# Kernel tuning notes

Measured on AMD Instinct MI355X. Metric: run time of the kernel, lower is better.

The kernel has to match this reference:

```python
import jax, jax.numpy as jnp
import numpy as np

H, DI, N, K, R, FF = 2048, 4096, 16, 4, 128, 5632
B, S = 2, 1024
EPS = 1e-6


def rmsnorm(x, w):
    v = jnp.mean(x * x, axis=-1, keepdims=True)
    return x * jax.lax.rsqrt(v + EPS) * w


def setup_inputs() -> dict:
    key = jax.random.key(0)
    ks = jax.random.split(key, 16)
    sc = 0.02
    inp = {
        "hidden_states": jax.random.normal(ks[0], (B, S, H), jnp.float32),
        "input_ln_w": jnp.ones((H,), jnp.float32),
        "w_in": jax.random.normal(ks[1], (2 * DI, H), jnp.float32) * sc,
        "conv_w": jax.random.normal(ks[2], (DI, 1, K), jnp.float32) * 0.3,
        "conv_b": jax.random.normal(ks[3], (DI,), jnp.float32) * sc,
        "w_x": jax.random.normal(ks[4], (R + 2 * N, DI), jnp.float32) * sc,
        "dt_ln_w": jnp.ones((R,), jnp.float32),
        "b_ln_w": jnp.ones((N,), jnp.float32),
        "c_ln_w": jnp.ones((N,), jnp.float32),
        "w_dt": jax.random.normal(ks[5], (DI, R), jnp.float32) * sc,
        "b_dt": jax.random.normal(ks[6], (DI,), jnp.float32) * sc - 4.0,
        "A_log": jnp.broadcast_to(jnp.log(jnp.arange(1, N + 1, dtype=jnp.float32)), (DI, N)),
        "D_skip": jnp.ones((DI,), jnp.float32),
        "w_out": jax.random.normal(ks[7], (H, DI), jnp.float32) * sc,
        "pre_ff_ln_w": jnp.ones((H,), jnp.float32),
        "w_gate": jax.random.normal(ks[8], (FF, H), jnp.float32) * sc,
        "w_up": jax.random.normal(ks[9], (FF, H), jnp.float32) * sc,
        "w_down": jax.random.normal(ks[10], (H, FF), jnp.float32) * sc,
    }
    return inp


def causal_conv1d(x, w, b):
    # x: [B,S,DI], w: [DI,1,K] depthwise, left-pad K-1 (causal)
    y = jax.lax.conv_general_dilated(
        x.transpose(0, 2, 1), w,
        window_strides=(1,), padding=[(K - 1, 0)],
        dimension_numbers=("NCH", "OIH", "NCH"),
        feature_group_count=DI)
    return (y + b[None, :, None]).transpose(0, 2, 1)


def selective_scan(u, A, Bm, Cm, Dp, dt):
    # u,dt: [B,S,DI]; A: [DI,N]; Bm,Cm: [B,S,N]
    def step(h, xs):
        dt_t, B_t, C_t, u_t = xs  # [B,DI],[B,N],[B,N],[B,DI]
        dA = jnp.exp(dt_t[:, :, None] * A)                      # [B,DI,N]
        dBu = dt_t[:, :, None] * B_t[:, None, :] * u_t[:, :, None]
        h = dA * h + dBu
        y = jnp.einsum("bdn,bn->bd", h, C_t)
        return h, y

    xs = (dt.transpose(1, 0, 2), Bm.transpose(1, 0, 2),
          Cm.transpose(1, 0, 2), u.transpose(1, 0, 2))
    h0 = jnp.zeros((u.shape[0], DI, N), u.dtype)
    _, ys = jax.lax.scan(step, h0, xs)
    return ys.transpose(1, 0, 2) + u * Dp  # [B,S,DI]


def reference(hidden_states, input_ln_w, w_in, conv_w, conv_b, w_x, dt_ln_w,
              b_ln_w, c_ln_w, w_dt, b_dt, A_log, D_skip, w_out, pre_ff_ln_w,
              w_gate, w_up, w_down):
    residual = hidden_states
    x = rmsnorm(hidden_states, input_ln_w)

    # --- Mamba mixer ---
    proj = x @ w_in.T                       # [B,S,2*DI]
    u, gate = jnp.split(proj, 2, axis=-1)
    u = jax.nn.silu(causal_conv1d(u, conv_w, conv_b))
    ssm_p = u @ w_x.T                       # [B,S,R+2N]
    t_r, Bm, Cm = jnp.split(ssm_p, [R, R + N], axis=-1)
    t_r = rmsnorm(t_r, dt_ln_w)
    Bm = rmsnorm(Bm, b_ln_w)
    Cm = rmsnorm(Cm, c_ln_w)
    dt = jax.nn.softplus(t_r @ w_dt.T + b_dt)  # [B,S,DI]
    A = -jnp.exp(A_log)
    y = selective_scan(u, A, Bm, Cm, D_skip, dt)
    y = y * jax.nn.silu(gate)
    mixer_out = y @ w_out.T                  # [B,S,H]

    hidden = residual + mixer_out
    residual = hidden
    h = rmsnorm(hidden, pre_ff_ln_w)
    ff = (jax.nn.silu(h @ w_gate.T) * (h @ w_up.T)) @ w_down.T
    return residual + ff
```

## Files before the change

### kernel.cpp

```cpp
#include <hip/hip_runtime.h>
#include <stdint.h>

#define H_   2048
#define DI_  4096
#define N_   16
#define K_   4
#define R_   128
#define FF_  5632
#define B_   2
#define S_   1024
#define MROWS (B_*S_)
#define PCH  16
#define CSTEPS (S_/PCH)

typedef float f32x4 __attribute__((ext_vector_type(4)));
typedef float f32x2 __attribute__((ext_vector_type(2)));
typedef __bf16 bf16x8 __attribute__((ext_vector_type(8)));

__device__ __forceinline__ unsigned short f2bf(float f) {
    union { float f; unsigned u; } v; v.f = f;
    unsigned r = v.u + 0x7fffu + ((v.u >> 16) & 1u);
    return (unsigned short)(r >> 16);
}

__device__ __forceinline__ void gload16(const void* g, void* lds) {
    __builtin_amdgcn_global_load_lds(
        (const __attribute__((address_space(1))) unsigned int*)(uintptr_t)g,
        (__attribute__((address_space(3))) unsigned int*)(unsigned int)(uintptr_t)lds,
        16, 0, 0);
}

__global__ __launch_bounds__(256, 2)
void gemm_bt(const unsigned short* __restrict__ A, const unsigned short* __restrict__ Bt,
             float* __restrict__ C, int M, int N, int K, int Kc)
{
    __shared__ __align__(16) unsigned short As[128 * 64];
    __shared__ __align__(16) unsigned short Bs[128 * 64];
    const int t = threadIdx.x;
    const int l = t & 63;
    const int wv = t >> 6;

    int nwg = gridDim.x * gridDim.y;
    int wg = blockIdx.y * gridDim.x + blockIdx.x;
    if ((nwg & 7) == 0) {
        int q = nwg >> 3;
        wg = (wg & 7) * q + (wg >> 3);
    }
    const int bx = wg % gridDim.x;
    const int by = wg / gridDim.x;
    const long m0 = (long)by * 128;
    const long n0 = (long)bx * 128;
    const int wm = (wv >> 1) * 64;
    const int wn = (wv & 1) * 64;
    const long kstart = (long)blockIdx.z * Kc;
    C += (long)blockIdx.z * M * (long)N;

    f32x4 acc[4][4] = {};

    const int tr = t >> 3;
    const int cs = (t & 7) ^ (tr & 7);
    const unsigned short* gA = A + (m0 + tr) * (long)K + kstart + cs * 8;
    const unsigned short* gB = Bt + (n0 + tr) * (long)K + kstart + cs * 8;
    const unsigned ldsbase = (unsigned)(t & 192) * 16;

    for (int kt = 0; kt < Kc; kt += 64) {
#pragma unroll
        for (int j = 0; j < 4; ++j) {
            gload16(gA + (long)j * 32 * K, (char*)As + j * 4096 + ldsbase);
            gload16(gB + (long)j * 32 * K, (char*)Bs + j * 4096 + ldsbase);
        }
        gA += 64; gB += 64;
        __syncthreads();
#pragma unroll
        for (int k0 = 0; k0 < 2; ++k0) {
            bf16x8 af[4], bfr[4];
#pragma unroll
            for (int i = 0; i < 4; ++i) {
                int rowa = wm + i * 16 + (l & 15);
                int ca = (k0 * 4 + (l >> 4)) ^ (rowa & 7);
                af[i] = *(const bf16x8*)(As + rowa * 64 + ca * 8);
                int rowb = wn + i * 16 + (l & 15);
                int cb = (k0 * 4 + (l >> 4)) ^ (rowb & 7);
                bfr[i] = *(const bf16x8*)(Bs + rowb * 64 + cb * 8);
            }
#pragma unroll
            for (int i = 0; i < 4; ++i)
#pragma unroll
                for (int jn = 0; jn < 4; ++jn)
                    acc[i][jn] = __builtin_amdgcn_mfma_f32_16x16x32_bf16(
                        af[i], bfr[jn], acc[i][jn], 0, 0, 0);
        }
        __syncthreads();
    }

    const int crow = (l >> 4) * 4;
    const int ccol = l & 15;
#pragma unroll
    for (int i = 0; i < 4; ++i) {
#pragma unroll
        for (int jn = 0; jn < 4; ++jn) {
            long row = m0 + wm + i * 16 + crow;
            long col = n0 + wn + jn * 16 + ccol;
            float* cp = C + row * (long)N + col;
#pragma unroll
            for (int q = 0; q < 4; ++q) cp[(long)q * N] = acc[i][jn][q];
        }
    }
}

__global__ __launch_bounds__(512, 1)
void gemm_bt256(const unsigned short* __restrict__ A, const unsigned short* __restrict__ Bt,
                float* __restrict__ C, int M, int N, int K, int Kc)
{
    __shared__ __align__(16) unsigned short As[2][256 * 64];
    __shared__ __align__(16) unsigned short Bs[2][256 * 64];
    const int t = threadIdx.x;
    const int l = t & 63;
    const int wv = t >> 6;
    const int wm = wv >> 2;
    const int wn = wv & 3;

    int nwg = gridDim.x * gridDim.y;
    int wg = blockIdx.y * gridDim.x + blockIdx.x;
    if ((nwg & 7) == 0) {
        int q = nwg >> 3;
        wg = (wg & 7) * q + (wg >> 3);
    }
    const int bx = wg % gridDim.x;
    const int by = wg / gridDim.x;
    const long m0 = (long)by * 256;
    const long n0 = (long)bx * 256;
    const long kstart = (long)blockIdx.z * Kc;
    C += (long)blockIdx.z * M * (long)N;

    f32x4 acc[8][4] = {};

    const int cs = (t & 7) ^ ((t >> 3) & 7);
    const unsigned short* gA = A + (m0 + (t >> 3)) * (long)K + kstart + cs * 8;
    const unsigned short* gB = Bt + (n0 + (t >> 3)) * (long)K + kstart + cs * 8;
    const int NT = Kc >> 6;

#pragma unroll
    for (int i = 0; i < 4; ++i)
        gload16(gA + (long)i * 64 * K, &As[0][t * 8 + i * 4096]);
#pragma unroll
    for (int i = 0; i < 4; ++i)
        gload16(gB + (long)i * 64 * K, &Bs[0][t * 8 + i * 4096]);

    for (int kt = 0; kt < NT; ++kt) {
        const int buf = kt & 1;
        const long koff = (long)((kt + 1 < NT) ? (kt + 1) : kt) * 64;
#pragma unroll
        for (int i = 0; i < 4; ++i)
            gload16(gA + koff + (long)i * 64 * K, &As[buf ^ 1][t * 8 + i * 4096]);
        asm volatile("s_waitcnt vmcnt(4)" ::: "memory");
        __builtin_amdgcn_sched_barrier(0);
        __builtin_amdgcn_s_barrier();
        __builtin_amdgcn_sched_barrier(0);
        {
            bf16x8 af[8], bfr[4];
#pragma unroll
            for (int nf = 0; nf < 4; ++nf) {
                int rowb = wn * 64 + nf * 16 + (l & 15);
                int cb = (l >> 4) ^ (rowb & 7);
                bfr[nf] = *(const bf16x8*)(&Bs[buf][rowb * 64 + cb * 8]);
            }
#pragma unroll
            for (int mf = 0; mf < 8; ++mf) {
                int rowa = wm * 128 + mf * 16 + (l & 15);
                int ca = (l >> 4) ^ (rowa & 7);
                af[mf] = *(const bf16x8*)(&As[buf][rowa * 64 + ca * 8]);
            }
            __builtin_amdgcn_s_setprio(1);
#pragma unroll
            for (int mf = 0; mf < 8; ++mf)
#pragma unroll
                for (int nf = 0; nf < 4; ++nf)
                    acc[mf][nf] = __builtin_amdgcn_mfma_f32_16x16x32_bf16(
                        af[mf], bfr[nf], acc[mf][nf], 0, 0, 0);
            __builtin_amdgcn_s_setprio(0);
        }
        __builtin_amdgcn_sched_barrier(0);
#pragma unroll
        for (int i = 0; i < 4; ++i)
            gload16(gB + koff + (long)i * 64 * K, &Bs[buf ^ 1][t * 8 + i * 4096]);
        {
            bf16x8 af[8], bfr[4];
#pragma unroll
            for (int nf = 0; nf < 4; ++nf) {
                int rowb = wn * 64 + nf * 16 + (l & 15);
                int cb = (4 + (l >> 4)) ^ (rowb & 7);
                bfr[nf] = *(const bf16x8*)(&Bs[buf][rowb * 64 + cb * 8]);
            }
#pragma unroll
            for (int mf = 0; mf < 8; ++mf) {
                int rowa = wm * 128 + mf * 16 + (l & 15);
                int ca = (4 + (l >> 4)) ^ (rowa & 7);
                af[mf] = *(const bf16x8*)(&As[buf][rowa * 64 + ca * 8]);
            }
            __builtin_amdgcn_s_setprio(1);
#pragma unroll
            for (int mf = 0; mf < 8; ++mf)
#pragma unroll
                for (int nf = 0; nf < 4; ++nf)
                    acc[mf][nf] = __builtin_amdgcn_mfma_f32_16x16x32_bf16(
                        af[mf], bfr[nf], acc[mf][nf], 0, 0, 0);
            __builtin_amdgcn_s_setprio(0);
        }
        __builtin_amdgcn_sched_barrier(0);
        __builtin_amdgcn_s_barrier();
        __builtin_amdgcn_sched_barrier(0);
    }

    const int crow = (l >> 4) * 4;
    const int ccol = l & 15;
#pragma unroll
    for (int mf = 0; mf < 8; ++mf) {
#pragma unroll
        for (int nf = 0; nf < 4; ++nf) {
            long row = m0 + wm * 128 + mf * 16 + crow;
            long col = n0 + wn * 64 + nf * 16 + ccol;
            float* cp = C + row * (long)N + col;
#pragma unroll
            for (int q = 0; q < 4; ++q) cp[(long)q * N] = acc[mf][nf][q];
        }
    }
}

__global__ __launch_bounds__(256)
void cvt_bf16(const float* __restrict__ x, unsigned short* __restrict__ y, long n)
{
    long i = ((long)blockIdx.x * 256 + threadIdx.x) * 4;
    if (i >= n) return;
    float4 v = *(const float4*)(x + i);
    ushort4 o;
    o.x = f2bf(v.x); o.y = f2bf(v.y); o.z = f2bf(v.z); o.w = f2bf(v.w);
    *(ushort4*)(y + i) = o;
}

__global__ __launch_bounds__(256)
void cvt_pad_wx(const float* __restrict__ x, unsigned short* __restrict__ y)
{
    long i = ((long)blockIdx.x * 256 + threadIdx.x) * 4;
    int row = (int)(i >> 12);
    ushort4 o;
    if (row < 160) {
        float4 v = *(const float4*)(x + i);
        o.x = f2bf(v.x); o.y = f2bf(v.y); o.z = f2bf(v.z); o.w = f2bf(v.w);
    } else { o.x = 0; o.y = 0; o.z = 0; o.w = 0; }
    *(ushort4*)(y + i) = o;
}

__global__ __launch_bounds__(256)
void rmsnorm_cast(const float* __restrict__ x, const float* __restrict__ w,
                  unsigned short* __restrict__ out)
{
    const long row = blockIdx.x;
    const float* xr = x + row * H_ + threadIdx.x * 8;
    float4 v0 = *(const float4*)xr;
    float4 v1 = *(const float4*)(xr + 4);
    float xv[8] = {v0.x, v0.y, v0.z, v0.w, v1.x, v1.y, v1.z, v1.w};
    float s = 0.f;
#pragma unroll
    for (int j = 0; j < 8; ++j) s += xv[j] * xv[j];
#pragma unroll
    for (int m = 32; m; m >>= 1) s += __shfl_xor(s, m);
    __shared__ float red[4];
    if ((threadIdx.x & 63) == 0) red[threadIdx.x >> 6] = s;
    __syncthreads();
    s = red[0] + red[1] + red[2] + red[3];
    float inv = rsqrtf(s * (1.f / H_) + 1e-6f);
    const float* wr = w + threadIdx.x * 8;
    unsigned short* op = out + row * H_ + threadIdx.x * 8;
    ushort4 o0, o1;
    o0.x = f2bf(xv[0] * inv * wr[0]); o0.y = f2bf(xv[1] * inv * wr[1]);
    o0.z = f2bf(xv[2] * inv * wr[2]); o0.w = f2bf(xv[3] * inv * wr[3]);
    o1.x = f2bf(xv[4] * inv * wr[4]); o1.y = f2bf(xv[5] * inv * wr[5]);
    o1.z = f2bf(xv[6] * inv * wr[6]); o1.w = f2bf(xv[7] * inv * wr[7]);
    *(ushort4*)op = o0;
    *(ushort4*)(op + 4) = o1;
}

__global__ __launch_bounds__(256)
void add_rmsnorm(const float* __restrict__ a, const float* __restrict__ mx,
                 const float* __restrict__ w, float* __restrict__ hid,
                 unsigned short* __restrict__ hb)
{
    const long row = blockIdx.x;
    const long off = row * H_ + threadIdx.x * 8;
    float xv[8];
    {
        float4 a0 = *(const float4*)(a + off);
        float4 a1 = *(const float4*)(a + off + 4);
        xv[0] = a0.x; xv[1] = a0.y; xv[2] = a0.z; xv[3] = a0.w;
        xv[4] = a1.x; xv[5] = a1.y; xv[6] = a1.z; xv[7] = a1.w;
    }
#pragma unroll
    for (int z = 0; z < 4; ++z) {
        const float* mz = mx + (long)z * MROWS * H_ + off;
        float4 b0 = *(const float4*)mz;
        float4 b1 = *(const float4*)(mz + 4);
        xv[0] += b0.x; xv[1] += b0.y; xv[2] += b0.z; xv[3] += b0.w;
        xv[4] += b1.x; xv[5] += b1.y; xv[6] += b1.z; xv[7] += b1.w;
    }
    float s = 0.f;
#pragma unroll
    for (int j = 0; j < 8; ++j) s += xv[j] * xv[j];
#pragma unroll
    for (int m = 32; m; m >>= 1) s += __shfl_xor(s, m);
    __shared__ float red[4];
    if ((threadIdx.x & 63) == 0) red[threadIdx.x >> 6] = s;
    __syncthreads();
    s = red[0] + red[1] + red[2] + red[3];
    float inv = rsqrtf(s * (1.f / H_) + 1e-6f);
    float4 h0, h1;
    h0.x = xv[0]; h0.y = xv[1]; h0.z = xv[2]; h0.w = xv[3];
    h1.x = xv[4]; h1.y = xv[5]; h1.z = xv[6]; h1.w = xv[7];
    *(float4*)(hid + off) = h0;
    *(float4*)(hid + off + 4) = h1;
    const float* wr = w + threadIdx.x * 8;
    ushort4 o0, o1;
    o0.x = f2bf(xv[0] * inv * wr[0]); o0.y = f2bf(xv[1] * inv * wr[1]);
    o0.z = f2bf(xv[2] * inv * wr[2]); o0.w = f2bf(xv[3] * inv * wr[3]);
    o1.x = f2bf(xv[4] * inv * wr[4]); o1.y = f2bf(xv[5] * inv * wr[5]);
    o1.z = f2bf(xv[6] * inv * wr[6]); o1.w = f2bf(xv[7] * inv * wr[7]);
    *(ushort4*)(hb + off) = o0;
    *(ushort4*)(hb + off + 4) = o1;
}

__global__ __launch_bounds__(256)
void conv_silu(const float* __restrict__ proj, const float* __restrict__ cw,
               const float* __restrict__ cb, float* __restrict__ uf,
               unsigned short* __restrict__ ub)
{
    long i = (long)blockIdx.x * 256 + threadIdx.x;
    int d = (int)(i & (DI_ - 1));
    long sd = i >> 12;
    int s = (int)(sd & (S_ - 1));
    long rb = sd * (2 * DI_) + d;
    float w0 = cw[d * 4], w1 = cw[d * 4 + 1], w2 = cw[d * 4 + 2], w3 = cw[d * 4 + 3];
    float acc = cb[d] + w3 * proj[rb];
    if (s >= 1) acc += w2 * proj[rb - 2 * DI_];
    if (s >= 2) acc += w1 * proj[rb - 4 * DI_];
    if (s >= 3) acc += w0 * proj[rb - 6 * DI_];
    float r = acc / (1.f + __expf(-acc));
    uf[i] = r;
    ub[i] = f2bf(r);
}

__global__ __launch_bounds__(256)
void ssm_norms(const float* __restrict__ ssmp, const float* __restrict__ wdt,
               const float* __restrict__ wb, const float* __restrict__ wc,
               unsigned short* __restrict__ trb, float* __restrict__ Bm,
               float* __restrict__ Cm)
{
    const long row = (long)blockIdx.x * 4 + (threadIdx.x >> 6);
    const int l = threadIdx.x & 63;
    float x0 = 0.f, x1 = 0.f, xb = 0.f, xc = 0.f;
#pragma unroll
    for (int z = 0; z < 8; ++z) {
        const float* rp = ssmp + (long)z * (MROWS * 256) + row * 256;
        x0 += rp[l];
        x1 += rp[64 + l];
        xb += rp[128 + (l & 15)];
        xc += rp[144 + (l & 15)];
    }
    float s = x0 * x0 + x1 * x1;
#pragma unroll
    for (int m = 32; m; m >>= 1) s += __shfl_xor(s, m);
    float inv = rsqrtf(s * (1.f / R_) + 1e-6f);
    trb[row * R_ + l] = f2bf(x0 * inv * wdt[l]);
    trb[row * R_ + 64 + l] = f2bf(x1 * inv * wdt[64 + l]);

    float sb = xb * xb, sc = xc * xc;
#pragma unroll
    for (int m = 8; m; m >>= 1) { sb += __shfl_xor(sb, m); sc += __shfl_xor(sc, m); }
    float invb = rsqrtf(sb * (1.f / N_) + 1e-6f);
    float invc = rsqrtf(sc * (1.f / N_) + 1e-6f);
    if (l < 16) {
        Bm[row * N_ + l] = xb * invb * wb[l];
        Cm[row * N_ + l] = xc * invc * wc[l];
    }
}

__global__ __launch_bounds__(256)
void softplus_bias(const float* __restrict__ x, const float* __restrict__ b,
                   float* __restrict__ y)
{
    long i = (long)blockIdx.x * 256 + threadIdx.x;
    int d = (int)(i & (DI_ - 1));
    float v = x[i] + b[d];
    y[i] = (v > 20.f) ? v : log1pf(__expf(v));
}


__global__ __launch_bounds__(64)
void scan_partA(const float* __restrict__ uf, const float* __restrict__ dt,
                const float* __restrict__ Bm, const float* __restrict__ A_log,
                float* __restrict__ TRH, float* __restrict__ TRS)
{
    __shared__ __align__(16) float UD[2][16][16][2];
    __shared__ __align__(16) float BB[2][16][16];

    const int l = threadIdx.x;
    const int ch = l & 15, sgx = l >> 4;
    const int dchunk = blockIdx.x >> 4;
    const int p = blockIdx.x & 15;
    const int gch0 = dchunk * 16;
    const int batch = gch0 >> 12;
    const int d0 = gch0 & (DI_ - 1);
    const int d = d0 + ch;
    const long bS = (long)batch * S_;
    const int t0 = p * CSTEPS;

    f32x4 Av;
    {
        f32x4 al = *(const f32x4*)&A_log[(long)d * N_ + sgx * 4];
        Av[0] = -__expf(al[0]); Av[1] = -__expf(al[1]);
        Av[2] = -__expf(al[2]); Av[3] = -__expf(al[3]);
    }
    const int sA = l >> 2;
    const int c4 = (l & 3) * 4;

    f32x4 u4, t4;
    {
        long row = bS + t0 + sA;
        u4 = *(const f32x4*)&uf[row * DI_ + d0 + c4];
        t4 = *(const f32x4*)&dt[row * DI_ + d0 + c4];
        gload16(Bm + (bS + t0) * N_ + l * 4, &BB[0][0][0]);
    }

    float h0 = 0.f, h1 = 0.f, h2 = 0.f, h3 = 0.f, sdt = 0.f;

    for (int ck = 0; ck < 4; ++ck) {
        const int buf = ck & 1;
        asm volatile("s_waitcnt vmcnt(0)" ::: "memory");
        __builtin_amdgcn_sched_barrier(0);
#pragma unroll
        for (int j = 0; j < 4; ++j) {
            f32x2 w; w[0] = t4[j]; w[1] = u4[j] * t4[j];
            *(f32x2*)&UD[buf][sA][c4 + j][0] = w;
        }
        if (ck + 1 < 4) {
            long row = bS + t0 + (ck + 1) * 16 + sA;
            u4 = *(const f32x4*)&uf[row * DI_ + d0 + c4];
            t4 = *(const f32x4*)&dt[row * DI_ + d0 + c4];
            gload16(Bm + (bS + t0 + (ck + 1) * 16) * N_ + l * 4, &BB[buf ^ 1][0][0]);
        }
#pragma unroll
        for (int s = 0; s < 16; ++s) {
            f32x2 dd = *(const f32x2*)&UD[buf][s][ch][0];
            f32x4 B4 = *(const f32x4*)&BB[buf][s][sgx * 4];
            float cdt = dd[0], dtu = dd[1];
            h0 = __expf(cdt * Av[0]) * h0 + dtu * B4[0];
            h1 = __expf(cdt * Av[1]) * h1 + dtu * B4[1];
            h2 = __expf(cdt * Av[2]) * h2 + dtu * B4[2];
            h3 = __expf(cdt * Av[3]) * h3 + dtu * B4[3];
            sdt += cdt;
        }
    }
    f32x4 hv; hv[0] = h0; hv[1] = h1; hv[2] = h2; hv[3] = h3;
    *(f32x4*)&TRH[((long)(gch0 + ch)) * (PCH * 16) + p * 16 + sgx * 4] = hv;
    if (l < 16) TRS[(gch0 + l) * PCH + p] = sdt;
}

__global__ __launch_bounds__(256)
void scan_combine(const float* __restrict__ A_log, const float* __restrict__ TRS,
                  float* __restrict__ TRH)
{
    const int tid = blockIdx.x * 256 + threadIdx.x;
    const int gch = tid >> 4, n = tid & 15;
    const int d = gch & (DI_ - 1);
    const float Av = -__expf(A_log[(long)d * N_ + n]);
    const float* sp = TRS + (long)gch * PCH;
    float* hp = TRH + (long)gch * (PCH * 16) + n;
    float h = 0.f;
#pragma unroll
    for (int p = 0; p < PCH; ++p) {
        float hl = hp[p * 16];
        float e = __expf(Av * sp[p]);
        hp[p * 16] = h;
        h = hl + e * h;
    }
}

__global__ __launch_bounds__(64)
void scan_partC(const float* __restrict__ uf, const float* __restrict__ dt,
                const float* __restrict__ Bm, const float* __restrict__ Cm,
                const float* __restrict__ A_log, const float* __restrict__ Dskip,
                const float* __restrict__ proj, const float* __restrict__ TRH,
                unsigned short* __restrict__ yb)
{
    __shared__ __align__(16) float UDG[2][16][16][4];
    __shared__ __align__(16) float BB[2][16][16];
    __shared__ __align__(16) float CC[2][16][16];

    const int l = threadIdx.x;
    const int ch = l & 15, sgx = l >> 4;
    const int dchunk = blockIdx.x >> 4;
    const int p = blockIdx.x & 15;
    const int gch0 = dchunk * 16;
    const int batch = gch0 >> 12;
    const int d0 = gch0 & (DI_ - 1);
    const int d = d0 + ch;
    const long bS = (long)batch * S_;
    const int t0 = p * CSTEPS;

    f32x4 Av;
    {
        f32x4 al = *(const f32x4*)&A_log[(long)d * N_ + sgx * 4];
        Av[0] = -__expf(al[0]); Av[1] = -__expf(al[1]);
        Av[2] = -__expf(al[2]); Av[3] = -__expf(al[3]);
    }
    const float Dv = Dskip[d];

    f32x4 hv = *(const f32x4*)&TRH[((long)(gch0 + ch)) * (PCH * 16) + p * 16 + sgx * 4];
    float h0 = hv[0], h1 = hv[1], h2 = hv[2], h3 = hv[3];

    const int sA = l >> 2;
    const int c4 = (l & 3) * 4;

    f32x4 u4, t4, g4;
    {
        long row = bS + t0 + sA;
        u4 = *(const f32x4*)&uf[row * DI_ + d0 + c4];
        t4 = *(const f32x4*)&dt[row * DI_ + d0 + c4];
        g4 = *(const f32x4*)&proj[row * (2L * DI_) + DI_ + d0 + c4];
        gload16(Bm + (bS + t0) * N_ + l * 4, &BB[0][0][0]);
        gload16(Cm + (bS + t0) * N_ + l * 4, &CC[0][0][0]);
    }

    for (int ck = 0; ck < 4; ++ck) {
        const int buf = ck & 1;
        asm volatile("s_waitcnt vmcnt(0)" ::: "memory");
        __builtin_amdgcn_sched_barrier(0);
#pragma unroll
        for (int j = 0; j < 4; ++j) {
            f32x4 w;
            w[0] = u4[j]; w[1] = t4[j]; w[2] = g4[j]; w[3] = u4[j] * t4[j];
            *(f32x4*)&UDG[buf][sA][c4 + j][0] = w;
        }
        if (ck + 1 < 4) {
            long row = bS + t0 + (ck + 1) * 16 + sA;
            u4 = *(const f32x4*)&uf[row * DI_ + d0 + c4];
            t4 = *(const f32x4*)&dt[row * DI_ + d0 + c4];
            g4 = *(const f32x4*)&proj[row * (2L * DI_) + DI_ + d0 + c4];
            gload16(Bm + (bS + t0 + (ck + 1) * 16) * N_ + l * 4, &BB[buf ^ 1][0][0]);
            gload16(Cm + (bS + t0 + (ck + 1) * 16) * N_ + l * 4, &CC[buf ^ 1][0][0]);
        }
#pragma unroll
        for (int s = 0; s < 16; ++s) {
            f32x4 udg = *(const f32x4*)&UDG[buf][s][ch][0];
            f32x4 B4 = *(const f32x4*)&BB[buf][s][sgx * 4];
            f32x4 C4 = *(const f32x4*)&CC[buf][s][sgx * 4];
            float cdt = udg[1], dtu = udg[3];
            h0 = __expf(cdt * Av[0]) * h0 + dtu * B4[0];
            h1 = __expf(cdt * Av[1]) * h1 + dtu * B4[1];
            h2 = __expf(cdt * Av[2]) * h2 + dtu * B4[2];
            h3 = __expf(cdt * Av[3]) * h3 + dtu * B4[3];
            float pr = (h0 * C4[0] + h1 * C4[1]) + (h2 * C4[2] + h3 * C4[3]);
            pr += __shfl_xor(pr, 16);
            pr += __shfl_xor(pr, 32);
            if (l < 16) {
                float y = pr + udg[0] * Dv;
                float cg = udg[2];
                float sl = cg / (1.f + __expf(-cg));
                yb[(bS + t0 + ck * 16 + s) * DI_ + d] = f2bf(y * sl);
            }
        }
    }
}

__global__ __launch_bounds__(256)
void silu_mul(const float* __restrict__ g, const float* __restrict__ u,
              unsigned short* __restrict__ out, long n)
{
    long i = ((long)blockIdx.x * 256 + threadIdx.x) * 4;
    if (i >= n) return;
    float4 gv = *(const float4*)(g + i);
    float4 uv = *(const float4*)(u + i);
    ushort4 o;
    o.x = f2bf(gv.x / (1.f + __expf(-gv.x)) * uv.x);
    o.y = f2bf(gv.y / (1.f + __expf(-gv.y)) * uv.y);
    o.z = f2bf(gv.z / (1.f + __expf(-gv.z)) * uv.z);
    o.w = f2bf(gv.w / (1.f + __expf(-gv.w)) * uv.w);
    *(ushort4*)(out + i) = o;
}

__global__ __launch_bounds__(256)
void final_add(const float* __restrict__ a, const float* __restrict__ b,
               float* __restrict__ y, long n)
{
    long i = ((long)blockIdx.x * 256 + threadIdx.x) * 4;
    if (i >= n) return;
    float4 av = *(const float4*)(a + i);
    float4 o = av;
#pragma unroll
    for (int z = 0; z < 4; ++z) {
        float4 bv = *(const float4*)(b + (long)z * MROWS * H_ + i);
        o.x += bv.x; o.y += bv.y; o.z += bv.z; o.w += bv.w;
    }
    *(float4*)(y + i) = o;
}

extern "C" void kernel_launch(void* const* d_in, const int* in_sizes, int n_in,
                              void* d_out, int out_size, void* d_ws, size_t ws_size,
                              hipStream_t stream)
{
    const float* hs     = (const float*)d_in[0];
    const float* ln_in  = (const float*)d_in[1];
    const float* w_in   = (const float*)d_in[2];
    const float* conv_w = (const float*)d_in[3];
    const float* conv_b = (const float*)d_in[4];
    const float* w_x    = (const float*)d_in[5];
    const float* dt_ln  = (const float*)d_in[6];
    const float* b_ln   = (const float*)d_in[7];
    const float* c_ln   = (const float*)d_in[8];
    const float* w_dt   = (const float*)d_in[9];
    const float* b_dt   = (const float*)d_in[10];
    const float* A_log  = (const float*)d_in[11];
    const float* Dskip  = (const float*)d_in[12];
    const float* w_out  = (const float*)d_in[13];
    const float* ln_ff  = (const float*)d_in[14];
    const float* w_gate = (const float*)d_in[15];
    const float* w_up   = (const float*)d_in[16];
    const float* w_down = (const float*)d_in[17];
    float* out = (float*)d_out;
    char* ws = (char*)d_ws;

    unsigned short* WB    = (unsigned short*)(ws + 0L);
    unsigned short* XB    = (unsigned short*)(ws + 33554432L);
    float*          PROJ  = (float*)(ws + 41943040L);
    float*          MIX   = (float*)(ws + 41943040L);
    float*          GF    = (float*)(ws + 41943040L);
    float*          FFT   = (float*)(ws + 41943040L);
    float*          UF    = (float*)(ws + 109051904L);
    unsigned short* FFACT = (unsigned short*)(ws + 109051904L);
    unsigned short* UB    = (unsigned short*)(ws + 142606336L);
    float*          HID   = (float*)(ws + 142606336L);
    unsigned short* TRB   = (unsigned short*)(ws + 159383552L);
    float*          BM    = (float*)(ws + 159907840L);
    float*          CM    = (float*)(ws + 160038912L);
    float*          TRS   = (float*)(ws + 160169984L);
    float*          SSMP  = (float*)(ws + 160694272L);
    float*          DTRAW = (float*)(ws + 160694272L);
    float*          TRH   = (float*)(ws + 160694272L);
    float*          DT    = (float*)(ws + 194248704L);
    float*          UPF   = (float*)(ws + 194248704L);
    unsigned short* YB    = (unsigned short*)(ws + 227803136L);
    unsigned short* HB    = XB;

    auto gemm = [&](const unsigned short* A, const unsigned short* Bt, float* C,
                    int M, int N, int K, int kch) {
        dim3 g(N / 128, M / 128, kch);
        gemm_bt<<<g, 256, 0, stream>>>(A, Bt, C, M, N, K, K / kch);
    };
    auto gemm256 = [&](const unsigned short* A, const unsigned short* Bt, float* C,
                       int M, int N, int K, int kch) {
        dim3 g(N / 256, M / 256, kch);
        gemm_bt256<<<g, 512, 0, stream>>>(A, Bt, C, M, N, K, K / kch);
    };
    auto cvt = [&](const float* x, unsigned short* y, long n) {
        cvt_bf16<<<(int)((n / 4 + 255) / 256), 256, 0, stream>>>(x, y, n);
    };

    cvt(w_in, WB, (long)2 * DI_ * H_);
    rmsnorm_cast<<<MROWS, 256, 0, stream>>>(hs, ln_in, XB);
    gemm256(XB, WB, PROJ, MROWS, 2 * DI_, H_, 1);
    conv_silu<<<(MROWS * DI_) / 256, 256, 0, stream>>>(PROJ, conv_w, conv_b, UF, UB);
    cvt_pad_wx<<<(256 * DI_ / 4) / 256, 256, 0, stream>>>(w_x, WB);
    gemm(UB, WB, SSMP, MROWS, 256, DI_, 8);
    ssm_norms<<<MROWS / 4, 256, 0, stream>>>(SSMP, dt_ln, b_ln, c_ln, TRB, BM, CM);
    cvt(w_dt, WB, (long)DI_ * R_);
    gemm(TRB, WB, DTRAW, MROWS, DI_, R_, 1);
    softplus_bias<<<(MROWS * DI_) / 256, 256, 0, stream>>>(DTRAW, b_dt, DT);
    scan_partA<<<(B_ * DI_ / 16) * PCH, 64, 0, stream>>>(UF, DT, BM, A_log, TRH, TRS);
    scan_combine<<<(B_ * DI_ * N_) / 256, 256, 0, stream>>>(A_log, TRS, TRH);
    scan_partC<<<(B_ * DI_ / 16) * PCH, 64, 0, stream>>>(UF, DT, BM, CM, A_log, Dskip,
                                                         PROJ, TRH, YB);
    cvt(w_out, WB, (long)H_ * DI_);
    gemm256(YB, WB, MIX, MROWS, H_, DI_, 4);
    add_rmsnorm<<<MROWS, 256, 0, stream>>>(hs, MIX, ln_ff, HID, HB);
    cvt(w_gate, WB, (long)FF_ * H_);
    gemm256(HB, WB, GF, MROWS, FF_, H_, 1);
    cvt(w_up, WB, (long)FF_ * H_);
    gemm256(HB, WB, UPF, MROWS, FF_, H_, 1);
    silu_mul<<<(int)(((long)MROWS * FF_ / 4 + 255) / 256), 256, 0, stream>>>(
        GF, UPF, FFACT, (long)MROWS * FF_);
    cvt(w_down, WB, (long)H_ * FF_);
    gemm256(FFACT, WB, FFT, MROWS, H_, FF_, 4);
    final_add<<<(int)(((long)MROWS * H_ / 4 + 255) / 256), 256, 0, stream>>>(
        HID, FFT, out, (long)MROWS * H_);
}
```

Measured before the change: 588.2 us.

## Fuse softplus bias into scan kernels and pack four scan tasks per block

Removes the standalone softplus_bias kernel and its full-size DT buffer, so both scan passes read raw dt-projection output and apply bias plus softplus inline. The scan kernels now run four independent 64-thread tasks per 256-thread block, each wave using its own LDS slice. B/C staging switches from async global_load_lds double buffering to register loads followed by LDS stores, and TRH moves to a region that no longer aliases DTRAW. This saves one write and one read of a 32 MB tensor and a launch, at the cost of computing softplus twice, once in each scan pass.

```diff
diff --git a/kernel.cpp b/kernel.cpp
--- a/kernel.cpp
+++ b/kernel.cpp
@@ -21,6 +21,10 @@
     union { float f; unsigned u; } v; v.f = f;
     unsigned r = v.u + 0x7fffu + ((v.u >> 16) & 1u);
     return (unsigned short)(r >> 16);
+}
+
+__device__ __forceinline__ float softplusf(float v) {
+    return (v > 20.f) ? v : log1pf(__expf(v));
 }
 
 __device__ __forceinline__ void gload16(const void* g, void* lds) {
@@ -383,29 +387,22 @@
     }
 }
 
-__global__ __launch_bounds__(256)
-void softplus_bias(const float* __restrict__ x, const float* __restrict__ b,
-                   float* __restrict__ y)
-{
-    long i = (long)blockIdx.x * 256 + threadIdx.x;
-    int d = (int)(i & (DI_ - 1));
-    float v = x[i] + b[d];
-    y[i] = (v > 20.f) ? v : log1pf(__expf(v));
-}
-
-
-__global__ __launch_bounds__(64)
-void scan_partA(const float* __restrict__ uf, const float* __restrict__ dt,
-                const float* __restrict__ Bm, const float* __restrict__ A_log,
+
+__global__ __launch_bounds__(256)
+void scan_partA(const float* __restrict__ uf, const float* __restrict__ dtraw,
+                const float* __restrict__ bdt, const float* __restrict__ Bm,
+                const float* __restrict__ A_log,
                 float* __restrict__ TRH, float* __restrict__ TRS)
 {
-    __shared__ __align__(16) float UD[2][16][16][2];
-    __shared__ __align__(16) float BB[2][16][16];
-
-    const int l = threadIdx.x;
+    __shared__ __align__(16) float UD[4][16][16][2];
+    __shared__ __align__(16) float BBs[4][16][16];
+
+    const int w = threadIdx.x >> 6;
+    const int l = threadIdx.x & 63;
     const int ch = l & 15, sgx = l >> 4;
-    const int dchunk = blockIdx.x >> 4;
-    const int p = blockIdx.x & 15;
+    const int task = blockIdx.x * 4 + w;
+    const int dchunk = task >> 4;
+    const int p = task & 15;
     const int gch0 = dchunk * 16;
     const int batch = gch0 >> 12;
     const int d0 = gch0 & (DI_ - 1);
@@ -421,36 +418,39 @@
     }
     const int sA = l >> 2;
     const int c4 = (l & 3) * 4;
-
-    f32x4 u4, t4;
+    const f32x4 bias4 = *(const f32x4*)&bdt[d0 + c4];
+
+    f32x4 u4, t4, b4;
     {
         long row = bS + t0 + sA;
         u4 = *(const f32x4*)&uf[row * DI_ + d0 + c4];
-        t4 = *(const f32x4*)&dt[row * DI_ + d0 + c4];
-        gload16(Bm + (bS + t0) * N_ + l * 4, &BB[0][0][0]);
+        f32x4 tr = *(const f32x4*)&dtraw[row * DI_ + d0 + c4];
+#pragma unroll
+        for (int j = 0; j < 4; ++j) t4[j] = softplusf(tr[j] + bias4[j]);
+        b4 = *(const f32x4*)&Bm[(bS + t0) * N_ + l * 4];
     }
 
     float h0 = 0.f, h1 = 0.f, h2 = 0.f, h3 = 0.f, sdt = 0.f;
 
     for (int ck = 0; ck < 4; ++ck) {
-        const int buf = ck & 1;
-        asm volatile("s_waitcnt vmcnt(0)" ::: "memory");
-        __builtin_amdgcn_sched_barrier(0);
 #pragma unroll
         for (int j = 0; j < 4; ++j) {
-            f32x2 w; w[0] = t4[j]; w[1] = u4[j] * t4[j];
-            *(f32x2*)&UD[buf][sA][c4 + j][0] = w;
-        }
+            f32x2 wv; wv[0] = t4[j]; wv[1] = u4[j] * t4[j];
+            *(f32x2*)&UD[w][sA][c4 + j][0] = wv;
+        }
+        *(f32x4*)((float*)&BBs[w][0][0] + l * 4) = b4;
         if (ck + 1 < 4) {
             long row = bS + t0 + (ck + 1) * 16 + sA;
             u4 = *(const f32x4*)&uf[row * DI_ + d0 + c4];
-            t4 = *(const f32x4*)&dt[row * DI_ + d0 + c4];
-            gload16(Bm + (bS + t0 + (ck + 1) * 16) * N_ + l * 4, &BB[buf ^ 1][0][0]);
+            f32x4 tr = *(const f32x4*)&dtraw[row * DI_ + d0 + c4];
+#pragma unroll
+            for (int j = 0; j < 4; ++j) t4[j] = softplusf(tr[j] + bias4[j]);
+            b4 = *(const f32x4*)&Bm[(bS + t0 + (ck + 1) * 16) * N_ + l * 4];
         }
 #pragma unroll
         for (int s = 0; s < 16; ++s) {
-            f32x2 dd = *(const f32x2*)&UD[buf][s][ch][0];
-            f32x4 B4 = *(const f32x4*)&BB[buf][s][sgx * 4];
+            f32x2 dd = *(const f32x2*)&UD[w][s][ch][0];
+            f32x4 B4 = *(const f32x4*)&BBs[w][s][sgx * 4];
             float cdt = dd[0], dtu = dd[1];
             h0 = __expf(cdt * Av[0]) * h0 + dtu * B4[0];
             h1 = __expf(cdt * Av[1]) * h1 + dtu * B4[1];
@@ -484,21 +484,23 @@
     }
 }
 
-__global__ __launch_bounds__(64)
-void scan_partC(const float* __restrict__ uf, const float* __restrict__ dt,
-                const float* __restrict__ Bm, const float* __restrict__ Cm,
-                const float* __restrict__ A_log, const float* __restrict__ Dskip,
-                const float* __restrict__ proj, const float* __restrict__ TRH,
-                unsigned short* __restrict__ yb)
-{
-    __shared__ __align__(16) float UDG[2][16][16][4];
-    __shared__ __align__(16) float BB[2][16][16];
-    __shared__ __align__(16) float CC[2][16][16];
-
-    const int l = threadIdx.x;
+__global__ __launch_bounds__(256)
+void scan_partC(const float* __restrict__ uf, const float* __restrict__ dtraw,
+                const float* __restrict__ bdt, const float* __restrict__ Bm,
+                const float* __restrict__ Cm, const float* __restrict__ A_log,
+                const float* __restrict__ Dskip, const float* __restrict__ proj,
+                const float* __restrict__ TRH, unsigned short* __restrict__ yb)
+{
+    __shared__ __align__(16) float UDG[4][16][16][4];
+    __shared__ __align__(16) float BBs[4][16][16];
+    __shared__ __align__(16) float CCs[4][16][16];
+
+    const int w = threadIdx.x >> 6;
+    const int l = threadIdx.x & 63;
     const int ch = l & 15, sgx = l >> 4;
-    const int dchunk = blockIdx.x >> 4;
-    const int p = blockIdx.x & 15;
+    const int task = blockIdx.x * 4 + w;
+    const int dchunk = task >> 4;
+    const int p = task & 15;
     const int gch0 = dchunk * 16;
     const int batch = gch0 >> 12;
     const int d0 = gch0 & (DI_ - 1);
@@ -519,40 +521,44 @@
 
     const int sA = l >> 2;
     const int c4 = (l & 3) * 4;
-
-    f32x4 u4, t4, g4;
+    const f32x4 bias4 = *(const f32x4*)&bdt[d0 + c4];
+
+    f32x4 u4, t4, g4, b4, c4v;
     {
         long row = bS + t0 + sA;
         u4 = *(const f32x4*)&uf[row * DI_ + d0 + c4];
-        t4 = *(const f32x4*)&dt[row * DI_ + d0 + c4];
+        f32x4 tr = *(const f32x4*)&dtraw[row * DI_ + d0 + c4];
+#pragma unroll
+        for (int j = 0; j < 4; ++j) t4[j] = softplusf(tr[j] + bias4[j]);
         g4 = *(const f32x4*)&proj[row * (2L * DI_) + DI_ + d0 + c4];
-        gload16(Bm + (bS + t0) * N_ + l * 4, &BB[0][0][0]);
-        gload16(Cm + (bS + t0) * N_ + l * 4, &CC[0][0][0]);
+        b4 = *(const f32x4*)&Bm[(bS + t0) * N_ + l * 4];
+        c4v = *(const f32x4*)&Cm[(bS + t0) * N_ + l * 4];
     }
 
     for (int ck = 0; ck < 4; ++ck) {
-        const int buf = ck & 1;
-        asm volatile("s_waitcnt vmcnt(0)" ::: "memory");
-        __builtin_amdgcn_sched_barrier(0);
 #pragma unroll
         for (int j = 0; j < 4; ++j) {
-            f32x4 w;
-            w[0] = u4[j]; w[1] = t4[j]; w[2] = g4[j]; w[3] = u4[j] * t4[j];
-            *(f32x4*)&UDG[buf][sA][c4 + j][0] = w;
-        }
+            f32x4 wv;
+            wv[0] = u4[j]; wv[1] = t4[j]; wv[2] = g4[j]; wv[3] = u4[j] * t4[j];
+            *(f32x4*)&UDG[w][sA][c4 + j][0] = wv;
+        }
+        *(f32x4*)((float*)&BBs[w][0][0] + l * 4) = b4;
+        *(f32x4*)((float*)&CCs[w][0][0] + l * 4) = c4v;
         if (ck + 1 < 4) {
             long row = bS + t0 + (ck + 1) * 16 + sA;
             u4 = *(const f32x4*)&uf[row * DI_ + d0 + c4];
-            t4 = *(const f32x4*)&dt[row * DI_ + d0 + c4];
+            f32x4 tr = *(const f32x4*)&dtraw[row * DI_ + d0 + c4];
+#pragma unroll
+            for (int j = 0; j < 4; ++j) t4[j] = softplusf(tr[j] + bias4[j]);
             g4 = *(const f32x4*)&proj[row * (2L * DI_) + DI_ + d0 + c4];
-            gload16(Bm + (bS + t0 + (ck + 1) * 16) * N_ + l * 4, &BB[buf ^ 1][0][0]);
-            gload16(Cm + (bS + t0 + (ck + 1) * 16) * N_ + l * 4, &CC[buf ^ 1][0][0]);
+            b4 = *(const f32x4*)&Bm[(bS + t0 + (ck + 1) * 16) * N_ + l * 4];
+            c4v = *(const f32x4*)&Cm[(bS + t0 + (ck + 1) * 16) * N_ + l * 4];
         }
 #pragma unroll
         for (int s = 0; s < 16; ++s) {
-            f32x4 udg = *(const f32x4*)&UDG[buf][s][ch][0];
-            f32x4 B4 = *(const f32x4*)&BB[buf][s][sgx * 4];
-            f32x4 C4 = *(const f32x4*)&CC[buf][s][sgx * 4];
+            f32x4 udg = *(const f32x4*)&UDG[w][s][ch][0];
+            f32x4 B4 = *(const f32x4*)&BBs[w][s][sgx * 4];
+            f32x4 C4 = *(const f32x4*)&CCs[w][s][sgx * 4];
             float cdt = udg[1], dtu = udg[3];
             h0 = __expf(cdt * Av[0]) * h0 + dtu * B4[0];
             h1 = __expf(cdt * Av[1]) * h1 + dtu * B4[1];
@@ -644,8 +650,7 @@
     float*          TRS   = (float*)(ws + 160169984L);
     float*          SSMP  = (float*)(ws + 160694272L);
     float*          DTRAW = (float*)(ws + 160694272L);
-    float*          TRH   = (float*)(ws + 160694272L);
-    float*          DT    = (float*)(ws + 194248704L);
+    float*          TRH   = (float*)(ws + 194248704L);
     float*          UPF   = (float*)(ws + 194248704L);
     unsigned short* YB    = (unsigned short*)(ws + 227803136L);
     unsigned short* HB    = XB;
@@ -673,11 +678,11 @@
     ssm_norms<<<MROWS / 4, 256, 0, stream>>>(SSMP, dt_ln, b_ln, c_ln, TRB, BM, CM);
     cvt(w_dt, WB, (long)DI_ * R_);
     gemm(TRB, WB, DTRAW, MROWS, DI_, R_, 1);
-    softplus_bias<<<(MROWS * DI_) / 256, 256, 0, stream>>>(DTRAW, b_dt, DT);
-    scan_partA<<<(B_ * DI_ / 16) * PCH, 64, 0, stream>>>(UF, DT, BM, A_log, TRH, TRS);
+    scan_partA<<<(B_ * DI_ / 16) * PCH / 4, 256, 0, stream>>>(UF, DTRAW, b_dt, BM,
+                                                              A_log, TRH, TRS);
     scan_combine<<<(B_ * DI_ * N_) / 256, 256, 0, stream>>>(A_log, TRS, TRH);
-    scan_partC<<<(B_ * DI_ / 16) * PCH, 64, 0, stream>>>(UF, DT, BM, CM, A_log, Dskip,
-                                                         PROJ, TRH, YB);
+    scan_partC<<<(B_ * DI_ / 16) * PCH / 4, 256, 0, stream>>>(UF, DTRAW, b_dt, BM, CM,
+                                                              A_log, Dskip, PROJ, TRH, YB);
     cvt(w_out, WB, (long)H_ * DI_);
     gemm256(YB, WB, MIX, MROWS, H_, DI_, 4);
     add_rmsnorm<<<MROWS, 256, 0, stream>>>(hs, MIX, ln_ff, HID, HB);
```

New measurement: 599.7 us. About the same (+2.0%).
